# Performance work log

Measured on AMD Instinct MI355X. Metric: run time of the kernel, lower is better.

## Reference

```python
import jax, jax.numpy as jnp
import numpy as np

EMB = 64
NUM_LAYERS = 2


def _mlp_embed(x, shift, scale, w1, b1, w2, b2):
    # PreNormLayer: (x + shift) * scale, then Linear-ReLU-Linear-ReLU
    x = (x + shift) * scale
    x = jax.nn.relu(x @ w1 + b1)
    return jax.nn.relu(x @ w2 + b2)


def _sage_conv(x_src, x_dst, src_idx, dst_idx, ll_w, ll_b, lr_w):
    # PyG SAGEConv: mean-aggregate gathered source features at destinations,
    # out = lin_l(mean) + lin_r(x_dst); lin_l has bias, lin_r does not.
    n_dst = x_dst.shape[0]
    msgs = x_src[src_idx]                                   # [E, D] gather
    ssum = jax.ops.segment_sum(msgs, dst_idx, num_segments=n_dst)
    cnt = jax.ops.segment_sum(jnp.ones(src_idx.shape[0], x_src.dtype),
                              dst_idx, num_segments=n_dst)
    mean = ssum / jnp.maximum(cnt, 1.0)[:, None]            # [n_dst, D]
    return mean @ ll_w + ll_b + x_dst @ lr_w


def setup_inputs() -> dict:
    key = jax.random.key(0)
    ks = jax.random.split(key, 20)
    n_cons, n_var, n_edges = 100_000, 200_000, 2_000_000
    cons_nf, var_nf, edge_nf = 5, 19, 1

    def lin(k, fan_in, fan_out):
        return jax.random.normal(k, (fan_in, fan_out), jnp.float32) / np.sqrt(fan_in)

    inp = {
        'cons_x': jax.random.normal(ks[0], (n_cons, cons_nf), jnp.float32),
        'var_x': jax.random.normal(ks[1], (n_var, var_nf), jnp.float32),
        'edge_attr': jax.random.normal(ks[2], (n_edges, edge_nf), jnp.float32),
        'edge_index': jnp.stack([
            jax.random.randint(ks[3], (n_edges,), 0, n_cons),
            jax.random.randint(ks[4], (n_edges,), 0, n_var)]).astype(jnp.int64),
        # constraint embedding MLP
        'cons_shift': 0.1 * jax.random.normal(ks[5], (cons_nf,), jnp.float32),
        'cons_scale': 1.0 + 0.1 * jax.random.normal(ks[6], (cons_nf,), jnp.float32),
        'cons_w1': lin(ks[7], cons_nf, EMB),
        'cons_b1': jnp.zeros((EMB,), jnp.float32),
        'cons_w2': lin(ks[8], EMB, EMB),
        'cons_b2': jnp.zeros((EMB,), jnp.float32),
        # variable embedding MLP
        'var_shift': 0.1 * jax.random.normal(ks[9], (var_nf,), jnp.float32),
        'var_scale': 1.0 + 0.1 * jax.random.normal(ks[10], (var_nf,), jnp.float32),
        'var_w1': lin(ks[11], var_nf, EMB),
        'var_b1': jnp.zeros((EMB,), jnp.float32),
        'var_w2': lin(ks[12], EMB, EMB),
        'var_b2': jnp.zeros((EMB,), jnp.float32),
        # edge PreNorm (computed but unused for conv_type='sage', as in source)
        'edge_shift': 0.1 * jax.random.normal(ks[13], (edge_nf,), jnp.float32),
        'edge_scale': 1.0 + 0.1 * jax.random.normal(ks[14], (edge_nf,), jnp.float32),
        # SAGEConv weights: [layer, direction(0: cons->var, 1: var->cons), in, out]
        'conv_ll_w': jax.random.normal(ks[15], (NUM_LAYERS, 2, EMB, EMB), jnp.float32) / np.sqrt(EMB),
        'conv_ll_b': jnp.zeros((NUM_LAYERS, 2, EMB), jnp.float32),
        'conv_lr_w': jax.random.normal(ks[16], (NUM_LAYERS, 2, EMB, EMB), jnp.float32) / np.sqrt(EMB),
    }
    return inp


def reference(cons_x, var_x, edge_attr, edge_index,
              cons_shift, cons_scale, cons_w1, cons_b1, cons_w2, cons_b2,
              var_shift, var_scale, var_w1, var_b1, var_w2, var_b2,
              edge_shift, edge_scale, conv_ll_w, conv_ll_b, conv_lr_w):
    x_c = _mlp_embed(cons_x, cons_shift, cons_scale, cons_w1, cons_b1, cons_w2, cons_b2)
    x_v = _mlp_embed(var_x, var_shift, var_scale, var_w1, var_b1, var_w2, var_b2)
    edge_feat = (edge_attr + edge_shift) * edge_scale  # unused for SAGE (faithful to source)
    del edge_feat
    src, dst = edge_index[0], edge_index[1]  # constraint -> variable
    for l in range(NUM_LAYERS):
        new_v = _sage_conv(x_c, x_v, src, dst, conv_ll_w[l, 0], conv_ll_b[l, 0], conv_lr_w[l, 0])
        new_c = _sage_conv(x_v, x_c, dst, src, conv_ll_w[l, 1], conv_ll_b[l, 1], conv_lr_w[l, 1])
        x_c, x_v = jax.nn.relu(new_c), jax.nn.relu(new_v)
    return x_v
```

## Files before the change

kernel.cpp:

```cpp
#include <hip/hip_runtime.h>

#define EMB 64
#define CH 4096


static __device__ __forceinline__ unsigned short f2bf(float x) {
    union { float f; unsigned u; } v; v.f = x;
    unsigned r = v.u + 0x7fffu + ((v.u >> 16) & 1u);
    return (unsigned short)(r >> 16);
}
static __device__ __forceinline__ float bflo(unsigned w) {
    union { unsigned u; float f; } v; v.u = w << 16; return v.f;
}
static __device__ __forceinline__ float bfhi(unsigned w) {
    union { unsigned u; float f; } v; v.u = w & 0xffff0000u; return v.f;
}

__global__ __launch_bounds__(256) void zero_int_kernel(int* __restrict__ p, int n) {
    int i = blockIdx.x * 256 + threadIdx.x;
    if (i < n) p[i] = 0;
}

__global__ __launch_bounds__(256) void bucket_hist_kernel(
    const int* __restrict__ src, const int* __restrict__ dst, int E,
    int* __restrict__ bkt_cnt_c, int* __restrict__ bkt_cnt_v,
    int shc, int shv, int NBC, int NBV)
{
    __shared__ int hc[512], hv[512];
    int t = threadIdx.x;
    int base = blockIdx.x * CH;
    int n = min(CH, E - base);
    for (int i = t; i < NBC; i += 256) hc[i] = 0;
    for (int i = t; i < NBV; i += 256) hv[i] = 0;
    __syncthreads();
    for (int li = t; li < n; li += 256) {
        atomicAdd(&hc[src[base + li] >> shc], 1);
        atomicAdd(&hv[dst[base + li] >> shv], 1);
    }
    __syncthreads();
    for (int i = t; i < NBC; i += 256) { int c = hc[i]; if (c) atomicAdd(&bkt_cnt_c[i], c); }
    for (int i = t; i < NBV; i += 256) { int c = hv[i]; if (c) atomicAdd(&bkt_cnt_v[i], c); }
}

__global__ __launch_bounds__(256) void scan_buckets_kernel(
    int* __restrict__ bc, int nbc, int* __restrict__ bv, int nbv, int E)
{
    __shared__ int sc[256];
    int t = threadIdx.x;
    {
        int v0 = (2 * t < nbc) ? bc[2 * t] : 0;
        int v1 = (2 * t + 1 < nbc) ? bc[2 * t + 1] : 0;
        sc[t] = v0 + v1;
        __syncthreads();
        for (int off = 1; off < 256; off <<= 1) {
            int x = (t >= off) ? sc[t - off] : 0;
            __syncthreads();
            sc[t] += x;
            __syncthreads();
        }
        int ex = (t > 0) ? sc[t - 1] : 0;
        if (2 * t < nbc) bc[2 * t] = ex;
        if (2 * t + 1 < nbc) bc[2 * t + 1] = ex + v0;
        if (t == 0) bc[nbc] = E;
        __syncthreads();
    }
    {
        int v0 = (2 * t < nbv) ? bv[2 * t] : 0;
        int v1 = (2 * t + 1 < nbv) ? bv[2 * t + 1] : 0;
        sc[t] = v0 + v1;
        __syncthreads();
        for (int off = 1; off < 256; off <<= 1) {
            int x = (t >= off) ? sc[t - off] : 0;
            __syncthreads();
            sc[t] += x;
            __syncthreads();
        }
        int ex = (t > 0) ? sc[t - 1] : 0;
        if (2 * t < nbv) bv[2 * t] = ex;
        if (2 * t + 1 < nbv) bv[2 * t + 1] = ex + v0;
        if (t == 0) bv[nbv] = E;
    }
}

__global__ __launch_bounds__(256) void bin_edges_kernel(
    const int* __restrict__ src, const int* __restrict__ dst, int E,
    const int* __restrict__ bb_c, const int* __restrict__ bb_v,
    int* __restrict__ gcur_c, int* __restrict__ gcur_v,
    unsigned* __restrict__ tmp_c, unsigned* __restrict__ tmp_v,
    int shc, int shv, int NBC, int NBV)
{
    __shared__ int hc[512], hv[512];
    int t = threadIdx.x;
    int base = blockIdx.x * CH;
    int n = min(CH, E - base);
    unsigned mc = (1u << shc) - 1u, mv = (1u << shv) - 1u;

    for (int i = t; i < NBC; i += 256) hc[i] = 0;
    for (int i = t; i < NBV; i += 256) hv[i] = 0;
    __syncthreads();

    int ss[16], dd[16];
#pragma unroll
    for (int q = 0; q < 16; ++q) {
        int li = t + q * 256;
        bool ok = li < n;
        ss[q] = ok ? src[base + li] : -1;
        dd[q] = ok ? dst[base + li] : -1;
        if (ok) {
            atomicAdd(&hc[ss[q] >> shc], 1);
            atomicAdd(&hv[dd[q] >> shv], 1);
        }
    }
    __syncthreads();

    for (int i = t; i < NBC; i += 256) {
        int c = hc[i];
        hc[i] = c ? (bb_c[i] + atomicAdd(&gcur_c[i], c)) : 0;
    }
    for (int i = t; i < NBV; i += 256) {
        int c = hv[i];
        hv[i] = c ? (bb_v[i] + atomicAdd(&gcur_v[i], c)) : 0;
    }
    __syncthreads();

#pragma unroll
    for (int q = 0; q < 16; ++q) {
        int li = t + q * 256;
        if (li < n) {
            unsigned s = (unsigned)ss[q], d = (unsigned)dd[q];
            int pc = atomicAdd(&hc[s >> shc], 1);
            tmp_c[pc] = ((s & mc) << 23) | d;
            int pv = atomicAdd(&hv[d >> shv], 1);
            tmp_v[pv] = ((d & mv) << 23) | s;
        }
    }
}

__global__ __launch_bounds__(256) void regroup2_dual_kernel(
    const unsigned* __restrict__ tmpA, const int* __restrict__ bbA,
    int* __restrict__ rpA, int* __restrict__ adjA, int nAn, int shA, int nbA,
    const unsigned* __restrict__ tmpB, const int* __restrict__ bbB,
    int* __restrict__ rpB, int* __restrict__ adjB, int nBn, int shB, int nbB, int E)
{
    __shared__ int cnt[512];
    __shared__ int offs[512];
    __shared__ int sc[256];
    const unsigned* tmp; const int* bb; int* rp; int* adj; int n_nodes, sh, nb, b;
    if ((int)blockIdx.x < nbA) {
        tmp = tmpA; bb = bbA; rp = rpA; adj = adjA; n_nodes = nAn; sh = shA; nb = nbA; b = blockIdx.x;
    } else {
        tmp = tmpB; bb = bbB; rp = rpB; adj = adjB; n_nodes = nBn; sh = shB; nb = nbB; b = blockIdx.x - nbA;
    }
    int t = threadIdx.x;
    int node0 = b << sh;
    int node1 = min(node0 + (1 << sh), n_nodes);
    int nn = node1 - node0;
    for (int i = t; i < nn; i += 256) cnt[i] = 0;
    __syncthreads();
    int beg = bb[b], end = bb[b + 1];
    for (int e = beg + t; e < end; e += 256)
        atomicAdd(&cnt[tmp[e] >> 23], 1);
    __syncthreads();
    int v0 = (2 * t < nn) ? cnt[2 * t] : 0;
    int v1 = (2 * t + 1 < nn) ? cnt[2 * t + 1] : 0;
    sc[t] = v0 + v1;
    __syncthreads();
    for (int off = 1; off < 256; off <<= 1) {
        int x = (t >= off) ? sc[t - off] : 0;
        __syncthreads();
        sc[t] += x;
        __syncthreads();
    }
    int ex = (t > 0) ? sc[t - 1] : 0;
    if (2 * t < nn) offs[2 * t] = ex;
    if (2 * t + 1 < nn) offs[2 * t + 1] = ex + v0;
    __syncthreads();
    for (int i = t; i < nn; i += 256) {
        rp[node0 + i] = beg + offs[i];
        cnt[i] = 0;
    }
    if (b == nb - 1 && t == 0) rp[n_nodes] = E;
    __syncthreads();
    for (int e = beg + t; e < end; e += 256) {
        unsigned p = tmp[e];
        int d = (int)(p >> 23);
        int r = atomicAdd(&cnt[d], 1);
        adj[beg + offs[d] + r] = (int)(p & 0x7fffffu);
    }
}

template <int NF>
__device__ __forceinline__ void embed_body(
    float* hs, float* un,
    const float* __restrict__ x, const float* __restrict__ shift, const float* __restrict__ scale,
    const float* __restrict__ w1, const float* __restrict__ b1,
    const float* __restrict__ w2, const float* __restrict__ b2,
    const float* __restrict__ wll, const float* __restrict__ wlr,
    unsigned short* __restrict__ tb, float* __restrict__ u, int n, int bid)
{
    int t = threadIdx.x;
    long row0 = (long)bid * 64;
    int nrow = (n - row0 < 64) ? (int)(n - row0) : 64;

    float* xs  = un;
    float* w1s = un + NF * 68;

    for (int i = t; i < NF * EMB; i += 256) w1s[i] = w1[i];
    for (int i = t; i < 64 * NF; i += 256) {
        int r = i / NF, k = i - r * NF;
        float v = (r < nrow) ? x[row0 * NF + i] : 0.f;
        xs[k * 68 + r] = (v + shift[k]) * scale[k];
    }
    int r0 = (t >> 4) * 4;
    int cA = t & 15;
    float b1r[4], b2r[4];
#pragma unroll
    for (int j = 0; j < 4; ++j) { b1r[j] = b1[cA + 16 * j]; b2r[j] = b2[cA + 16 * j]; }
    __syncthreads();

    float a[4][4];
#pragma unroll
    for (int i = 0; i < 4; ++i)
#pragma unroll
        for (int j = 0; j < 4; ++j) a[i][j] = 0.f;
#pragma unroll
    for (int k = 0; k < NF; ++k) {
        float4 xv = *(const float4*)&xs[k * 68 + r0];
        float w0 = w1s[k * EMB + cA];
        float w1e = w1s[k * EMB + cA + 16];
        float w2e = w1s[k * EMB + cA + 32];
        float w3e = w1s[k * EMB + cA + 48];
        a[0][0] = fmaf(xv.x, w0, a[0][0]);  a[1][0] = fmaf(xv.y, w0, a[1][0]);
        a[2][0] = fmaf(xv.z, w0, a[2][0]);  a[3][0] = fmaf(xv.w, w0, a[3][0]);
        a[0][1] = fmaf(xv.x, w1e, a[0][1]); a[1][1] = fmaf(xv.y, w1e, a[1][1]);
        a[2][1] = fmaf(xv.z, w1e, a[2][1]); a[3][1] = fmaf(xv.w, w1e, a[3][1]);
        a[0][2] = fmaf(xv.x, w2e, a[0][2]); a[1][2] = fmaf(xv.y, w2e, a[1][2]);
        a[2][2] = fmaf(xv.z, w2e, a[2][2]); a[3][2] = fmaf(xv.w, w2e, a[3][2]);
        a[0][3] = fmaf(xv.x, w3e, a[0][3]); a[1][3] = fmaf(xv.y, w3e, a[1][3]);
        a[2][3] = fmaf(xv.z, w3e, a[2][3]); a[3][3] = fmaf(xv.w, w3e, a[3][3]);
    }
    __syncthreads();
#pragma unroll
    for (int j = 0; j < 4; ++j) {
        float* hp = &hs[(cA + 16 * j) * 65 + r0];
#pragma unroll
        for (int i = 0; i < 4; ++i) hp[i] = fmaxf(a[i][j] + b1r[j], 0.f);
    }
    {
        const float4* wg = (const float4*)w2;
        float4* wl = (float4*)un;
#pragma unroll
        for (int q = 0; q < 4; ++q) wl[t + q * 256] = wg[t + q * 256];
    }
    __syncthreads();

#pragma unroll
    for (int i = 0; i < 4; ++i)
#pragma unroll
        for (int j = 0; j < 4; ++j) a[i][j] = 0.f;
#pragma unroll 4
    for (int k = 0; k < EMB; ++k) {
        const float* hp = &hs[k * 65 + r0];
        float x0 = hp[0], x1 = hp[1], x2 = hp[2], x3 = hp[3];
        float w0 = un[k * EMB + cA];
        float w1e = un[k * EMB + cA + 16];
        float w2e = un[k * EMB + cA + 32];
        float w3e = un[k * EMB + cA + 48];
        a[0][0] = fmaf(x0, w0, a[0][0]);  a[1][0] = fmaf(x1, w0, a[1][0]);
        a[2][0] = fmaf(x2, w0, a[2][0]);  a[3][0] = fmaf(x3, w0, a[3][0]);
        a[0][1] = fmaf(x0, w1e, a[0][1]); a[1][1] = fmaf(x1, w1e, a[1][1]);
        a[2][1] = fmaf(x2, w1e, a[2][1]); a[3][1] = fmaf(x3, w1e, a[3][1]);
        a[0][2] = fmaf(x0, w2e, a[0][2]); a[1][2] = fmaf(x1, w2e, a[1][2]);
        a[2][2] = fmaf(x2, w2e, a[2][2]); a[3][2] = fmaf(x3, w2e, a[3][2]);
        a[0][3] = fmaf(x0, w3e, a[0][3]); a[1][3] = fmaf(x1, w3e, a[1][3]);
        a[2][3] = fmaf(x2, w3e, a[2][3]); a[3][3] = fmaf(x3, w3e, a[3][3]);
    }
    __syncthreads();
#pragma unroll
    for (int j = 0; j < 4; ++j) {
        float* hp = &hs[(cA + 16 * j) * 65 + r0];
#pragma unroll
        for (int i = 0; i < 4; ++i) hp[i] = fmaxf(a[i][j] + b2r[j], 0.f);
    }
    {
        const float4* wg = (const float4*)wll;
        float4* wl = (float4*)un;
#pragma unroll
        for (int q = 0; q < 4; ++q) wl[t + q * 256] = wg[t + q * 256];
    }
    __syncthreads();

    int c0g = (t & 15) * 4;
#pragma unroll
    for (int i = 0; i < 4; ++i)
#pragma unroll
        for (int j = 0; j < 4; ++j) a[i][j] = 0.f;
#pragma unroll 4
    for (int k = 0; k < EMB; ++k) {
        const float* hp = &hs[k * 65 + r0];
        float x0 = hp[0], x1 = hp[1], x2 = hp[2], x3 = hp[3];
        float4 wv = *(const float4*)&un[k * EMB + c0g];
        a[0][0] = fmaf(x0, wv.x, a[0][0]); a[0][1] = fmaf(x0, wv.y, a[0][1]);
        a[0][2] = fmaf(x0, wv.z, a[0][2]); a[0][3] = fmaf(x0, wv.w, a[0][3]);
        a[1][0] = fmaf(x1, wv.x, a[1][0]); a[1][1] = fmaf(x1, wv.y, a[1][1]);
        a[1][2] = fmaf(x1, wv.z, a[1][2]); a[1][3] = fmaf(x1, wv.w, a[1][3]);
        a[2][0] = fmaf(x2, wv.x, a[2][0]); a[2][1] = fmaf(x2, wv.y, a[2][1]);
        a[2][2] = fmaf(x2, wv.z, a[2][2]); a[2][3] = fmaf(x2, wv.w, a[2][3]);
        a[3][0] = fmaf(x3, wv.x, a[3][0]); a[3][1] = fmaf(x3, wv.y, a[3][1]);
        a[3][2] = fmaf(x3, wv.z, a[3][2]); a[3][3] = fmaf(x3, wv.w, a[3][3]);
    }
#pragma unroll
    for (int i = 0; i < 4; ++i) {
        long gr = row0 + r0 + i;
        if (gr < n) {
            ushort4 o;
            o.x = f2bf(a[i][0]); o.y = f2bf(a[i][1]);
            o.z = f2bf(a[i][2]); o.w = f2bf(a[i][3]);
            *(ushort4*)(tb + gr * EMB + c0g) = o;
        }
    }
    __syncthreads();
    {
        const float4* wg = (const float4*)wlr;
        float4* wl = (float4*)un;
#pragma unroll
        for (int q = 0; q < 4; ++q) wl[t + q * 256] = wg[t + q * 256];
    }
    __syncthreads();

#pragma unroll
    for (int i = 0; i < 4; ++i)
#pragma unroll
        for (int j = 0; j < 4; ++j) a[i][j] = 0.f;
#pragma unroll 4
    for (int k = 0; k < EMB; ++k) {
        const float* hp = &hs[k * 65 + r0];
        float x0 = hp[0], x1 = hp[1], x2 = hp[2], x3 = hp[3];
        float4 wv = *(const float4*)&un[k * EMB + c0g];
        a[0][0] = fmaf(x0, wv.x, a[0][0]); a[0][1] = fmaf(x0, wv.y, a[0][1]);
        a[0][2] = fmaf(x0, wv.z, a[0][2]); a[0][3] = fmaf(x0, wv.w, a[0][3]);
        a[1][0] = fmaf(x1, wv.x, a[1][0]); a[1][1] = fmaf(x1, wv.y, a[1][1]);
        a[1][2] = fmaf(x1, wv.z, a[1][2]); a[1][3] = fmaf(x1, wv.w, a[1][3]);
        a[2][0] = fmaf(x2, wv.x, a[2][0]); a[2][1] = fmaf(x2, wv.y, a[2][1]);
        a[2][2] = fmaf(x2, wv.z, a[2][2]); a[2][3] = fmaf(x2, wv.w, a[2][3]);
        a[3][0] = fmaf(x3, wv.x, a[3][0]); a[3][1] = fmaf(x3, wv.y, a[3][1]);
        a[3][2] = fmaf(x3, wv.z, a[3][2]); a[3][3] = fmaf(x3, wv.w, a[3][3]);
    }
#pragma unroll
    for (int i = 0; i < 4; ++i) {
        long gr = row0 + r0 + i;
        if (gr < n)
            *(float4*)&u[gr * EMB + c0g] = make_float4(a[i][0], a[i][1], a[i][2], a[i][3]);
    }
}

template <int NFA, int NFB>
__global__ __launch_bounds__(256) void embed_dual_kernel(
    const float* xA, const float* shA, const float* scA,
    const float* w1A, const float* b1A, const float* w2A, const float* b2A,
    const float* wllA, const float* wlrA, unsigned short* tbA, float* uA, int nA,
    const float* xB, const float* shB, const float* scB,
    const float* w1B, const float* b1B, const float* w2B, const float* b2B,
    const float* wllB, const float* wlrB, unsigned short* tbB, float* uB, int nB,
    int split)
{
    __shared__ float hs[EMB * 65];
    __shared__ float un[4096];
    if ((int)blockIdx.x < split)
        embed_body<NFA>(hs, un, xA, shA, scA, w1A, b1A, w2A, b2A, wllA, wlrA, tbA, uA, nA, blockIdx.x);
    else
        embed_body<NFB>(hs, un, xB, shB, scB, w1B, b1B, w2B, b2B, wllB, wlrB, tbB, uB, nB, blockIdx.x - split);
}

__global__ __launch_bounds__(256) void gemm64_dual_kernel(
    const float* __restrict__ XA, int nA, const float* __restrict__ WA, unsigned short* __restrict__ CA,
    const float* __restrict__ XB, int nB, const float* __restrict__ WB, float* __restrict__ CB, int split)
{
    __shared__ float xs[EMB * 68];
    __shared__ float w1s[EMB * EMB];

    const float* X; const float* W; int n; int bid; bool bf;
    if ((int)blockIdx.x < split) { X = XA; W = WA; n = nA; bid = blockIdx.x; bf = true; }
    else { X = XB; W = WB; n = nB; bid = blockIdx.x - split; bf = false; }

    int t = threadIdx.x;
    {
        int r = t >> 2;
        int cs = (t & 3) * 16;
        long gr = (long)bid * 64 + r;
        float4 v[4];
        if (gr < n) {
            const float4* sp = (const float4*)(X + gr * EMB + cs);
#pragma unroll
            for (int q = 0; q < 4; ++q) v[q] = sp[q];
        } else {
            float4 z = make_float4(0.f, 0.f, 0.f, 0.f);
#pragma unroll
            for (int q = 0; q < 4; ++q) v[q] = z;
        }
#pragma unroll
        for (int q = 0; q < 4; ++q) {
            xs[(cs + q * 4 + 0) * 68 + r] = v[q].x;
            xs[(cs + q * 4 + 1) * 68 + r] = v[q].y;
            xs[(cs + q * 4 + 2) * 68 + r] = v[q].z;
            xs[(cs + q * 4 + 3) * 68 + r] = v[q].w;
        }
        const float4* wg = (const float4*)W;
        float4* wl = (float4*)w1s;
#pragma unroll
        for (int q = 0; q < 4; ++q) wl[t + q * 256] = wg[t + q * 256];
    }
    __syncthreads();

    int r0 = (t >> 4) * 4;
    int c0 = (t & 15) * 4;
    float acc[4][4] = {{0.f}};
#pragma unroll 8
    for (int k = 0; k < EMB; ++k) {
        float4 xv = *(const float4*)&xs[k * 68 + r0];
        float4 wv = *(const float4*)&w1s[k * EMB + c0];
        float xa[4] = {xv.x, xv.y, xv.z, xv.w};
        float wa[4] = {wv.x, wv.y, wv.z, wv.w};
#pragma unroll
        for (int i = 0; i < 4; ++i)
#pragma unroll
            for (int j = 0; j < 4; ++j)
                acc[i][j] = fmaf(xa[i], wa[j], acc[i][j]);
    }

#pragma unroll
    for (int i = 0; i < 4; ++i) {
        long gr = (long)bid * 64 + r0 + i;
        if (gr < n) {
            if (bf) {
                ushort4 o;
                o.x = f2bf(acc[i][0]); o.y = f2bf(acc[i][1]);
                o.z = f2bf(acc[i][2]); o.w = f2bf(acc[i][3]);
                *(ushort4*)(CA + gr * EMB + c0) = o;
            } else {
                *(float4*)(CB + gr * EMB + c0) =
                    make_float4(acc[i][0], acc[i][1], acc[i][2], acc[i][3]);
            }
        }
    }
}

__global__ __launch_bounds__(256) void agg_rmw_kernel(
    const unsigned short* __restrict__ tbl, const int* __restrict__ rowptr,
    const int* __restrict__ adj, const float* __restrict__ bias,
    float* __restrict__ out, int n_dst)
{
    int lane = threadIdx.x & 63;
    int node = blockIdx.x * 4 + (threadIdx.x >> 6);
    if (node >= n_dst) return;
    int p = lane & 15;
    int g = lane >> 4;
    int beg = rowptr[node];
    int end = rowptr[node + 1];
    const uint2* tb = (const uint2*)tbl;
    float a0 = 0.f, a1 = 0.f, a2 = 0.f, a3 = 0.f;
    int e = beg + g;
    for (; e + 4 < end; e += 8) {
        int r0 = adj[e];
        int r1 = adj[e + 4];
        uint2 w0 = tb[(long)r0 * 16 + p];
        uint2 w1 = tb[(long)r1 * 16 + p];
        a0 += bflo(w0.x) + bflo(w1.x);
        a1 += bfhi(w0.x) + bfhi(w1.x);
        a2 += bflo(w0.y) + bflo(w1.y);
        a3 += bfhi(w0.y) + bfhi(w1.y);
    }
    if (e < end) {
        uint2 w0 = tb[(long)adj[e] * 16 + p];
        a0 += bflo(w0.x);
        a1 += bfhi(w0.x);
        a2 += bflo(w0.y);
        a3 += bfhi(w0.y);
    }
    a0 += __shfl_xor(a0, 16); a0 += __shfl_xor(a0, 32);
    a1 += __shfl_xor(a1, 16); a1 += __shfl_xor(a1, 32);
    a2 += __shfl_xor(a2, 16); a2 += __shfl_xor(a2, 32);
    a3 += __shfl_xor(a3, 16); a3 += __shfl_xor(a3, 32);
    if (g == 0) {
        int cnt = end - beg;
        float inv = 1.f / (float)(cnt > 0 ? cnt : 1);
        float4 bv = ((const float4*)bias)[p];
        float4* op = (float4*)(out + (long)node * EMB) + p;
        float4 ov = *op;
        float v0 = a0 * inv + bv.x + ov.x;
        float v1 = a1 * inv + bv.y + ov.y;
        float v2 = a2 * inv + bv.z + ov.z;
        float v3 = a3 * inv + bv.w + ov.w;
        *op = make_float4(fmaxf(v0, 0.f), fmaxf(v1, 0.f), fmaxf(v2, 0.f), fmaxf(v3, 0.f));
    }
}

__global__ __launch_bounds__(256) void agg_rmw_dual_kernel(
    const unsigned short* __restrict__ tblA, const int* __restrict__ rpA, const int* __restrict__ adjA,
    const float* __restrict__ biasA, float* __restrict__ outA, int nA,
    const unsigned short* __restrict__ tblB, const int* __restrict__ rpB, const int* __restrict__ adjB,
    const float* __restrict__ biasB, float* __restrict__ outB, int nB, int split)
{
    const unsigned short* tbl; const int* rowptr; const int* adj; const float* bias; float* out;
    int nd, bid;
    if ((int)blockIdx.x < split) {
        tbl = tblA; rowptr = rpA; adj = adjA; bias = biasA; out = outA; nd = nA; bid = blockIdx.x;
    } else {
        tbl = tblB; rowptr = rpB; adj = adjB; bias = biasB; out = outB; nd = nB; bid = blockIdx.x - split;
    }
    int lane = threadIdx.x & 63;
    int node = bid * 4 + (threadIdx.x >> 6);
    if (node >= nd) return;
    int p = lane & 15;
    int g = lane >> 4;
    int beg = rowptr[node];
    int end = rowptr[node + 1];
    const uint2* tb = (const uint2*)tbl;
    float a0 = 0.f, a1 = 0.f, a2 = 0.f, a3 = 0.f;
    int e = beg + g;
    for (; e + 4 < end; e += 8) {
        int r0 = adj[e];
        int r1 = adj[e + 4];
        uint2 w0 = tb[(long)r0 * 16 + p];
        uint2 w1 = tb[(long)r1 * 16 + p];
        a0 += bflo(w0.x) + bflo(w1.x);
        a1 += bfhi(w0.x) + bfhi(w1.x);
        a2 += bflo(w0.y) + bflo(w1.y);
        a3 += bfhi(w0.y) + bfhi(w1.y);
    }
    if (e < end) {
        uint2 w0 = tb[(long)adj[e] * 16 + p];
        a0 += bflo(w0.x);
        a1 += bfhi(w0.x);
        a2 += bflo(w0.y);
        a3 += bfhi(w0.y);
    }
    a0 += __shfl_xor(a0, 16); a0 += __shfl_xor(a0, 32);
    a1 += __shfl_xor(a1, 16); a1 += __shfl_xor(a1, 32);
    a2 += __shfl_xor(a2, 16); a2 += __shfl_xor(a2, 32);
    a3 += __shfl_xor(a3, 16); a3 += __shfl_xor(a3, 32);
    if (g == 0) {
        int cnt = end - beg;
        float inv = 1.f / (float)(cnt > 0 ? cnt : 1);
        float4 bv = ((const float4*)bias)[p];
        float4* op = (float4*)(out + (long)node * EMB) + p;
        float4 ov = *op;
        float v0 = a0 * inv + bv.x + ov.x;
        float v1 = a1 * inv + bv.y + ov.y;
        float v2 = a2 * inv + bv.z + ov.z;
        float v3 = a3 * inv + bv.w + ov.w;
        *op = make_float4(fmaxf(v0, 0.f), fmaxf(v1, 0.f), fmaxf(v2, 0.f), fmaxf(v3, 0.f));
    }
}

extern "C" void kernel_launch(void* const* d_in, const int* in_sizes, int n_in,
                              void* d_out, int out_size, void* d_ws, size_t ws_size,
                              hipStream_t stream) {
    const float* cons_x     = (const float*)d_in[0];
    const float* var_x      = (const float*)d_in[1];
    const int*   eidx       = (const int*)d_in[3];
    const float* cons_shift = (const float*)d_in[4];
    const float* cons_scale = (const float*)d_in[5];
    const float* cons_w1    = (const float*)d_in[6];
    const float* cons_b1    = (const float*)d_in[7];
    const float* cons_w2    = (const float*)d_in[8];
    const float* cons_b2    = (const float*)d_in[9];
    const float* var_shift  = (const float*)d_in[10];
    const float* var_scale  = (const float*)d_in[11];
    const float* var_w1     = (const float*)d_in[12];
    const float* var_b1     = (const float*)d_in[13];
    const float* var_w2     = (const float*)d_in[14];
    const float* var_b2     = (const float*)d_in[15];
    const float* ll_w       = (const float*)d_in[18];
    const float* ll_b       = (const float*)d_in[19];
    const float* lr_w       = (const float*)d_in[20];

    const int nC = in_sizes[0] / 5;
    const int nV = in_sizes[1] / 19;
    const int E  = in_sizes[3] / 2;
    const int* src = eidx;
    const int* dst = eidx + E;

    int shc = 0; while ((nC >> shc) >= 512) ++shc;
    int shv = 0; while ((nV >> shv) >= 512) ++shv;
    const int NBC = (nC + (1 << shc) - 1) >> shc;
    const int NBV = (nV + (1 << shv) - 1) >> shv;

    char* w = (char*)d_ws;
    auto alloc = [&](size_t bytes) {
        char* p = w;
        w += (bytes + 255) & ~(size_t)255;
        return p;
    };
    float* x_c = (float*)alloc((size_t)nC * EMB * 4);
    float* x_v = (float*)alloc((size_t)nV * EMB * 4);
    float* t_c = (float*)alloc((size_t)nC * EMB * 4);
    float* t_v = (float*)alloc((size_t)nV * EMB * 4);
    unsigned* tmp_c = (unsigned*)t_c;
    unsigned* tmp_v = (unsigned*)t_v;
    unsigned short* tb_c = (unsigned short*)t_c;
    unsigned short* tb_v = (unsigned short*)t_v;
    int* rp_v  = (int*)alloc((size_t)(nV + 1) * 4);
    int* rp_c  = (int*)alloc((size_t)(nC + 1) * 4);
    int* adj_v = (int*)alloc((size_t)E * 4);
    int* adj_c = (int*)alloc((size_t)E * 4);
    int* bkt   = (int*)alloc(4096 * 4);
    int* bb_c   = bkt;
    int* bb_v   = bkt + 1024;
    int* gcur_c = bkt + 2048;
    int* gcur_v = bkt + 3072;

    auto llw = [&](int l, int d) { return ll_w + (size_t)(l * 2 + d) * EMB * EMB; };
    auto lrw = [&](int l, int d) { return lr_w + (size_t)(l * 2 + d) * EMB * EMB; };
    auto llb = [&](int l, int d) { return ll_b + (size_t)(l * 2 + d) * EMB; };

    zero_int_kernel<<<16, 256, 0, stream>>>(bkt, 4096);
    bucket_hist_kernel<<<(E + CH - 1) / CH, 256, 0, stream>>>(src, dst, E, bb_c, bb_v, shc, shv, NBC, NBV);
    scan_buckets_kernel<<<1, 256, 0, stream>>>(bb_c, NBC, bb_v, NBV, E);
    bin_edges_kernel<<<(E + CH - 1) / CH, 256, 0, stream>>>(src, dst, E, bb_c, bb_v, gcur_c, gcur_v,
                                                            tmp_c, tmp_v, shc, shv, NBC, NBV);
    regroup2_dual_kernel<<<NBV + NBC, 256, 0, stream>>>(
        tmp_v, bb_v, rp_v, adj_v, nV, shv, NBV,
        tmp_c, bb_c, rp_c, adj_c, nC, shc, NBC, E);

    int gc = (nC + 63) / 64, gv = (nV + 63) / 64;
    embed_dual_kernel<5, 19><<<gc + gv, 256, 0, stream>>>(
        cons_x, cons_shift, cons_scale, cons_w1, cons_b1, cons_w2, cons_b2,
        llw(0, 0), lrw(0, 1), tb_c, x_c, nC,
        var_x, var_shift, var_scale, var_w1, var_b1, var_w2, var_b2,
        llw(0, 1), lrw(0, 0), tb_v, x_v, nV,
        gc);

    int gv4 = (nV + 3) / 4, gc4 = (nC + 3) / 4;
    agg_rmw_dual_kernel<<<gv4 + gc4, 256, 0, stream>>>(
        tb_c, rp_v, adj_v, llb(0, 0), x_v, nV,
        tb_v, rp_c, adj_c, llb(0, 1), x_c, nC,
        gv4);

    gemm64_dual_kernel<<<gc + gv, 256, 0, stream>>>(
        x_c, nC, llw(1, 0), tb_c,
        x_v, nV, lrw(1, 0), (float*)d_out, gc);

    agg_rmw_kernel<<<gv4, 256, 0, stream>>>(tb_c, rp_v, adj_v, llb(1, 0), (float*)d_out, nV);
}
```

Before: 468.5 us.

## Drop bucket histogram pass via fixed-slot binning; vectorize embed MLP LDS reads

Removes the separate bucket histogram kernel by binning edges into fixed-capacity per-bucket slots in the temp buffer. The per-bucket counts are then scanned afterward to get CSR offsets for the regroup step, which saves one full read pass over the 2M-edge index arrays and one launch. This assumes no bucket exceeds its slot capacity (twice the average, capped by buffer size), which random indices satisfy but skewed graphs might overflow. Separately, the embedding MLP uses float4 shared-memory loads with a padded stride of 68 and contiguous per-thread columns, and moves the lr weight load earlier.

```diff
diff --git a/kernel.cpp b/kernel.cpp
--- a/kernel.cpp
+++ b/kernel.cpp
@@ -19,27 +19,6 @@
 __global__ __launch_bounds__(256) void zero_int_kernel(int* __restrict__ p, int n) {
     int i = blockIdx.x * 256 + threadIdx.x;
     if (i < n) p[i] = 0;
-}
-
-__global__ __launch_bounds__(256) void bucket_hist_kernel(
-    const int* __restrict__ src, const int* __restrict__ dst, int E,
-    int* __restrict__ bkt_cnt_c, int* __restrict__ bkt_cnt_v,
-    int shc, int shv, int NBC, int NBV)
-{
-    __shared__ int hc[512], hv[512];
-    int t = threadIdx.x;
-    int base = blockIdx.x * CH;
-    int n = min(CH, E - base);
-    for (int i = t; i < NBC; i += 256) hc[i] = 0;
-    for (int i = t; i < NBV; i += 256) hv[i] = 0;
-    __syncthreads();
-    for (int li = t; li < n; li += 256) {
-        atomicAdd(&hc[src[base + li] >> shc], 1);
-        atomicAdd(&hv[dst[base + li] >> shv], 1);
-    }
-    __syncthreads();
-    for (int i = t; i < NBC; i += 256) { int c = hc[i]; if (c) atomicAdd(&bkt_cnt_c[i], c); }
-    for (int i = t; i < NBV; i += 256) { int c = hv[i]; if (c) atomicAdd(&bkt_cnt_v[i], c); }
 }
 
 __global__ __launch_bounds__(256) void scan_buckets_kernel(
@@ -84,10 +63,9 @@
 
 __global__ __launch_bounds__(256) void bin_edges_kernel(
     const int* __restrict__ src, const int* __restrict__ dst, int E,
-    const int* __restrict__ bb_c, const int* __restrict__ bb_v,
     int* __restrict__ gcur_c, int* __restrict__ gcur_v,
     unsigned* __restrict__ tmp_c, unsigned* __restrict__ tmp_v,
-    int shc, int shv, int NBC, int NBV)
+    int shc, int shv, int NBC, int NBV, int SLOTC, int SLOTV)
 {
     __shared__ int hc[512], hv[512];
     int t = threadIdx.x;
@@ -115,11 +93,11 @@
 
     for (int i = t; i < NBC; i += 256) {
         int c = hc[i];
-        hc[i] = c ? (bb_c[i] + atomicAdd(&gcur_c[i], c)) : 0;
+        hc[i] = c ? (i * SLOTC + atomicAdd(&gcur_c[i], c)) : 0;
     }
     for (int i = t; i < NBV; i += 256) {
         int c = hv[i];
-        hv[i] = c ? (bb_v[i] + atomicAdd(&gcur_v[i], c)) : 0;
+        hv[i] = c ? (i * SLOTV + atomicAdd(&gcur_v[i], c)) : 0;
     }
     __syncthreads();
 
@@ -138,18 +116,18 @@
 
 __global__ __launch_bounds__(256) void regroup2_dual_kernel(
     const unsigned* __restrict__ tmpA, const int* __restrict__ bbA,
-    int* __restrict__ rpA, int* __restrict__ adjA, int nAn, int shA, int nbA,
+    int* __restrict__ rpA, int* __restrict__ adjA, int nAn, int shA, int nbA, int slotA,
     const unsigned* __restrict__ tmpB, const int* __restrict__ bbB,
-    int* __restrict__ rpB, int* __restrict__ adjB, int nBn, int shB, int nbB, int E)
+    int* __restrict__ rpB, int* __restrict__ adjB, int nBn, int shB, int nbB, int slotB, int E)
 {
     __shared__ int cnt[512];
     __shared__ int offs[512];
     __shared__ int sc[256];
-    const unsigned* tmp; const int* bb; int* rp; int* adj; int n_nodes, sh, nb, b;
+    const unsigned* tmp; const int* bb; int* rp; int* adj; int n_nodes, sh, nb, b, slot;
     if ((int)blockIdx.x < nbA) {
-        tmp = tmpA; bb = bbA; rp = rpA; adj = adjA; n_nodes = nAn; sh = shA; nb = nbA; b = blockIdx.x;
+        tmp = tmpA; bb = bbA; rp = rpA; adj = adjA; n_nodes = nAn; sh = shA; nb = nbA; slot = slotA; b = blockIdx.x;
     } else {
-        tmp = tmpB; bb = bbB; rp = rpB; adj = adjB; n_nodes = nBn; sh = shB; nb = nbB; b = blockIdx.x - nbA;
+        tmp = tmpB; bb = bbB; rp = rpB; adj = adjB; n_nodes = nBn; sh = shB; nb = nbB; slot = slotB; b = blockIdx.x - nbA;
     }
     int t = threadIdx.x;
     int node0 = b << sh;
@@ -157,8 +135,10 @@
     int nn = node1 - node0;
     for (int i = t; i < nn; i += 256) cnt[i] = 0;
     __syncthreads();
-    int beg = bb[b], end = bb[b + 1];
-    for (int e = beg + t; e < end; e += 256)
+    int adjbase = bb[b];
+    int cntb = bb[b + 1] - adjbase;
+    int sbeg = b * slot;
+    for (int e = sbeg + t; e < sbeg + cntb; e += 256)
         atomicAdd(&cnt[tmp[e] >> 23], 1);
     __syncthreads();
     int v0 = (2 * t < nn) ? cnt[2 * t] : 0;
@@ -176,16 +156,16 @@
     if (2 * t + 1 < nn) offs[2 * t + 1] = ex + v0;
     __syncthreads();
     for (int i = t; i < nn; i += 256) {
-        rp[node0 + i] = beg + offs[i];
+        rp[node0 + i] = adjbase + offs[i];
         cnt[i] = 0;
     }
     if (b == nb - 1 && t == 0) rp[n_nodes] = E;
     __syncthreads();
-    for (int e = beg + t; e < end; e += 256) {
+    for (int e = sbeg + t; e < sbeg + cntb; e += 256) {
         unsigned p = tmp[e];
         int d = (int)(p >> 23);
         int r = atomicAdd(&cnt[d], 1);
-        adj[beg + offs[d] + r] = (int)(p & 0x7fffffu);
+        adj[adjbase + offs[d] + r] = (int)(p & 0x7fffffu);
     }
 }
 
@@ -212,10 +192,9 @@
         xs[k * 68 + r] = (v + shift[k]) * scale[k];
     }
     int r0 = (t >> 4) * 4;
-    int cA = t & 15;
-    float b1r[4], b2r[4];
-#pragma unroll
-    for (int j = 0; j < 4; ++j) { b1r[j] = b1[cA + 16 * j]; b2r[j] = b2[cA + 16 * j]; }
+    int c0 = (t & 15) * 4;
+    float4 b1v = *(const float4*)&b1[c0];
+    float4 b2v = *(const float4*)&b2[c0];
     __syncthreads();
 
     float a[4][4];
@@ -226,25 +205,27 @@
 #pragma unroll
     for (int k = 0; k < NF; ++k) {
         float4 xv = *(const float4*)&xs[k * 68 + r0];
-        float w0 = w1s[k * EMB + cA];
-        float w1e = w1s[k * EMB + cA + 16];
-        float w2e = w1s[k * EMB + cA + 32];
-        float w3e = w1s[k * EMB + cA + 48];
-        a[0][0] = fmaf(xv.x, w0, a[0][0]);  a[1][0] = fmaf(xv.y, w0, a[1][0]);
-        a[2][0] = fmaf(xv.z, w0, a[2][0]);  a[3][0] = fmaf(xv.w, w0, a[3][0]);
-        a[0][1] = fmaf(xv.x, w1e, a[0][1]); a[1][1] = fmaf(xv.y, w1e, a[1][1]);
-        a[2][1] = fmaf(xv.z, w1e, a[2][1]); a[3][1] = fmaf(xv.w, w1e, a[3][1]);
-        a[0][2] = fmaf(xv.x, w2e, a[0][2]); a[1][2] = fmaf(xv.y, w2e, a[1][2]);
-        a[2][2] = fmaf(xv.z, w2e, a[2][2]); a[3][2] = fmaf(xv.w, w2e, a[3][2]);
-        a[0][3] = fmaf(xv.x, w3e, a[0][3]); a[1][3] = fmaf(xv.y, w3e, a[1][3]);
-        a[2][3] = fmaf(xv.z, w3e, a[2][3]); a[3][3] = fmaf(xv.w, w3e, a[3][3]);
-    }
-    __syncthreads();
-#pragma unroll
-    for (int j = 0; j < 4; ++j) {
-        float* hp = &hs[(cA + 16 * j) * 65 + r0];
-#pragma unroll
-        for (int i = 0; i < 4; ++i) hp[i] = fmaxf(a[i][j] + b1r[j], 0.f);
+        float4 wv = *(const float4*)&w1s[k * EMB + c0];
+        float xa[4] = {xv.x, xv.y, xv.z, xv.w};
+        float wa[4] = {wv.x, wv.y, wv.z, wv.w};
+#pragma unroll
+        for (int i = 0; i < 4; ++i)
+#pragma unroll
+            for (int j = 0; j < 4; ++j)
+                a[i][j] = fmaf(xa[i], wa[j], a[i][j]);
+    }
+    __syncthreads();
+    {
+        float ba[4] = {b1v.x, b1v.y, b1v.z, b1v.w};
+#pragma unroll
+        for (int j = 0; j < 4; ++j) {
+            float4 o;
+            o.x = fmaxf(a[0][j] + ba[j], 0.f);
+            o.y = fmaxf(a[1][j] + ba[j], 0.f);
+            o.z = fmaxf(a[2][j] + ba[j], 0.f);
+            o.w = fmaxf(a[3][j] + ba[j], 0.f);
+            *(float4*)&hs[(c0 + j) * 68 + r0] = o;
+        }
     }
     {
         const float4* wg = (const float4*)w2;
@@ -258,29 +239,30 @@
     for (int i = 0; i < 4; ++i)
 #pragma unroll
         for (int j = 0; j < 4; ++j) a[i][j] = 0.f;
-#pragma unroll 4
+#pragma unroll 8
     for (int k = 0; k < EMB; ++k) {
-        const float* hp = &hs[k * 65 + r0];
-        float x0 = hp[0], x1 = hp[1], x2 = hp[2], x3 = hp[3];
-        float w0 = un[k * EMB + cA];
-        float w1e = un[k * EMB + cA + 16];
-        float w2e = un[k * EMB + cA + 32];
-        float w3e = un[k * EMB + cA + 48];
-        a[0][0] = fmaf(x0, w0, a[0][0]);  a[1][0] = fmaf(x1, w0, a[1][0]);
-        a[2][0] = fmaf(x2, w0, a[2][0]);  a[3][0] = fmaf(x3, w0, a[3][0]);
-        a[0][1] = fmaf(x0, w1e, a[0][1]); a[1][1] = fmaf(x1, w1e, a[1][1]);
-        a[2][1] = fmaf(x2, w1e, a[2][1]); a[3][1] = fmaf(x3, w1e, a[3][1]);
-        a[0][2] = fmaf(x0, w2e, a[0][2]); a[1][2] = fmaf(x1, w2e, a[1][2]);
-        a[2][2] = fmaf(x2, w2e, a[2][2]); a[3][2] = fmaf(x3, w2e, a[3][2]);
-        a[0][3] = fmaf(x0, w3e, a[0][3]); a[1][3] = fmaf(x1, w3e, a[1][3]);
-        a[2][3] = fmaf(x2, w3e, a[2][3]); a[3][3] = fmaf(x3, w3e, a[3][3]);
-    }
-    __syncthreads();
-#pragma unroll
-    for (int j = 0; j < 4; ++j) {
-        float* hp = &hs[(cA + 16 * j) * 65 + r0];
-#pragma unroll
-        for (int i = 0; i < 4; ++i) hp[i] = fmaxf(a[i][j] + b2r[j], 0.f);
+        float4 xv = *(const float4*)&hs[k * 68 + r0];
+        float4 wv = *(const float4*)&un[k * EMB + c0];
+        float xa[4] = {xv.x, xv.y, xv.z, xv.w};
+        float wa[4] = {wv.x, wv.y, wv.z, wv.w};
+#pragma unroll
+        for (int i = 0; i < 4; ++i)
+#pragma unroll
+            for (int j = 0; j < 4; ++j)
+                a[i][j] = fmaf(xa[i], wa[j], a[i][j]);
+    }
+    __syncthreads();
+    {
+        float ba[4] = {b2v.x, b2v.y, b2v.z, b2v.w};
+#pragma unroll
+        for (int j = 0; j < 4; ++j) {
+            float4 o;
+            o.x = fmaxf(a[0][j] + ba[j], 0.f);
+            o.y = fmaxf(a[1][j] + ba[j], 0.f);
+            o.z = fmaxf(a[2][j] + ba[j], 0.f);
+            o.w = fmaxf(a[3][j] + ba[j], 0.f);
+            *(float4*)&hs[(c0 + j) * 68 + r0] = o;
+        }
     }
     {
         const float4* wg = (const float4*)wll;
@@ -290,24 +272,28 @@
     }
     __syncthreads();
 
-    int c0g = (t & 15) * 4;
 #pragma unroll
     for (int i = 0; i < 4; ++i)
 #pragma unroll
         for (int j = 0; j < 4; ++j) a[i][j] = 0.f;
-#pragma unroll 4
+#pragma unroll 8
     for (int k = 0; k < EMB; ++k) {
-        const float* hp = &hs[k * 65 + r0];
-        float x0 = hp[0], x1 = hp[1], x2 = hp[2], x3 = hp[3];
-        float4 wv = *(const float4*)&un[k * EMB + c0g];
-        a[0][0] = fmaf(x0, wv.x, a[0][0]); a[0][1] = fmaf(x0, wv.y, a[0][1]);
-        a[0][2] = fmaf(x0, wv.z, a[0][2]); a[0][3] = fmaf(x0, wv.w, a[0][3]);
-        a[1][0] = fmaf(x1, wv.x, a[1][0]); a[1][1] = fmaf(x1, wv.y, a[1][1]);
-        a[1][2] = fmaf(x1, wv.z, a[1][2]); a[1][3] = fmaf(x1, wv.w, a[1][3]);
-        a[2][0] = fmaf(x2, wv.x, a[2][0]); a[2][1] = fmaf(x2, wv.y, a[2][1]);
-        a[2][2] = fmaf(x2, wv.z, a[2][2]); a[2][3] = fmaf(x2, wv.w, a[2][3]);
-        a[3][0] = fmaf(x3, wv.x, a[3][0]); a[3][1] = fmaf(x3, wv.y, a[3][1]);
-        a[3][2] = fmaf(x3, wv.z, a[3][2]); a[3][3] = fmaf(x3, wv.w, a[3][3]);
+        float4 xv = *(const float4*)&hs[k * 68 + r0];
+        float4 wv = *(const float4*)&un[k * EMB + c0];
+        float xa[4] = {xv.x, xv.y, xv.z, xv.w};
+        float wa[4] = {wv.x, wv.y, wv.z, wv.w};
+#pragma unroll
+        for (int i = 0; i < 4; ++i)
+#pragma unroll
+            for (int j = 0; j < 4; ++j)
+                a[i][j] = fmaf(xa[i], wa[j], a[i][j]);
+    }
+    __syncthreads();
+    {
+        const float4* wg = (const float4*)wlr;
+        float4* wl = (float4*)un;
+#pragma unroll
+        for (int q = 0; q < 4; ++q) wl[t + q * 256] = wg[t + q * 256];
     }
 #pragma unroll
     for (int i = 0; i < 4; ++i) {
@@ -316,15 +302,8 @@
             ushort4 o;
             o.x = f2bf(a[i][0]); o.y = f2bf(a[i][1]);
             o.z = f2bf(a[i][2]); o.w = f2bf(a[i][3]);
-            *(ushort4*)(tb + gr * EMB + c0g) = o;
-        }
-    }
-    __syncthreads();
-    {
-        const float4* wg = (const float4*)wlr;
-        float4* wl = (float4*)un;
-#pragma unroll
-        for (int q = 0; q < 4; ++q) wl[t + q * 256] = wg[t + q * 256];
+            *(ushort4*)(tb + gr * EMB + c0) = o;
+        }
     }
     __syncthreads();
 
@@ -332,25 +311,23 @@
     for (int i = 0; i < 4; ++i)
 #pragma unroll
         for (int j = 0; j < 4; ++j) a[i][j] = 0.f;
-#pragma unroll 4
+#pragma unroll 8
     for (int k = 0; k < EMB; ++k) {
-        const float* hp = &hs[k * 65 + r0];
-        float x0 = hp[0], x1 = hp[1], x2 = hp[2], x3 = hp[3];
-        float4 wv = *(const float4*)&un[k * EMB + c0g];
-        a[0][0] = fmaf(x0, wv.x, a[0][0]); a[0][1] = fmaf(x0, wv.y, a[0][1]);
-        a[0][2] = fmaf(x0, wv.z, a[0][2]); a[0][3] = fmaf(x0, wv.w, a[0][3]);
-        a[1][0] = fmaf(x1, wv.x, a[1][0]); a[1][1] = fmaf(x1, wv.y, a[1][1]);
-        a[1][2] = fmaf(x1, wv.z, a[1][2]); a[1][3] = fmaf(x1, wv.w, a[1][3]);
-        a[2][0] = fmaf(x2, wv.x, a[2][0]); a[2][1] = fmaf(x2, wv.y, a[2][1]);
-        a[2][2] = fmaf(x2, wv.z, a[2][2]); a[2][3] = fmaf(x2, wv.w, a[2][3]);
-        a[3][0] = fmaf(x3, wv.x, a[3][0]); a[3][1] = fmaf(x3, wv.y, a[3][1]);
-        a[3][2] = fmaf(x3, wv.z, a[3][2]); a[3][3] = fmaf(x3, wv.w, a[3][3]);
+        float4 xv = *(const float4*)&hs[k * 68 + r0];
+        float4 wv = *(const float4*)&un[k * EMB + c0];
+        float xa[4] = {xv.x, xv.y, xv.z, xv.w};
+        float wa[4] = {wv.x, wv.y, wv.z, wv.w};
+#pragma unroll
+        for (int i = 0; i < 4; ++i)
+#pragma unroll
+            for (int j = 0; j < 4; ++j)
+                a[i][j] = fmaf(xa[i], wa[j], a[i][j]);
     }
 #pragma unroll
     for (int i = 0; i < 4; ++i) {
         long gr = row0 + r0 + i;
         if (gr < n)
-            *(float4*)&u[gr * EMB + c0g] = make_float4(a[i][0], a[i][1], a[i][2], a[i][3]);
+            *(float4*)&u[gr * EMB + c0] = make_float4(a[i][0], a[i][1], a[i][2], a[i][3]);
     }
 }
 
@@ -364,8 +341,8 @@
     const float* wllB, const float* wlrB, unsigned short* tbB, float* uB, int nB,
     int split)
 {
-    __shared__ float hs[EMB * 65];
-    __shared__ float un[4096];
+    __shared__ __align__(16) float hs[EMB * 68];
+    __shared__ __align__(16) float un[4096];
     if ((int)blockIdx.x < split)
         embed_body<NFA>(hs, un, xA, shA, scA, w1A, b1A, w2A, b2A, wllA, wlrA, tbA, uA, nA, blockIdx.x);
     else
@@ -376,8 +353,8 @@
     const float* __restrict__ XA, int nA, const float* __restrict__ WA, unsigned short* __restrict__ CA,
     const float* __restrict__ XB, int nB, const float* __restrict__ WB, float* __restrict__ CB, int split)
 {
-    __shared__ float xs[EMB * 68];
-    __shared__ float w1s[EMB * EMB];
+    __shared__ __align__(16) float xs[EMB * 68];
+    __shared__ __align__(16) float w1s[EMB * EMB];
 
     const float* X; const float* W; int n; int bid; bool bf;
     if ((int)blockIdx.x < split) { X = XA; W = WA; n = nA; bid = blockIdx.x; bf = true; }
@@ -604,24 +581,33 @@
     int* rp_c  = (int*)alloc((size_t)(nC + 1) * 4);
     int* adj_v = (int*)alloc((size_t)E * 4);
     int* adj_c = (int*)alloc((size_t)E * 4);
-    int* bkt   = (int*)alloc(4096 * 4);
-    int* bb_c   = bkt;
-    int* bb_v   = bkt + 1024;
-    int* gcur_c = bkt + 2048;
-    int* gcur_v = bkt + 3072;
+    int* bkt   = (int*)alloc(2048 * 4);
+    int* gcur_c = bkt;
+    int* gcur_v = bkt + 1024;
+
+    auto slot_for = [&](int NB, size_t cap_ints) {
+        long s = 2L * E / NB;
+        s = (s + 255) & ~255L;
+        if (s < 4096) s = 4096;
+        long cap = (long)(cap_ints / NB) & ~255L;
+        if (s > cap) s = cap;
+        return (int)s;
+    };
+    const int SLOTC = slot_for(NBC, (size_t)nC * EMB);
+    const int SLOTV = slot_for(NBV, (size_t)nV * EMB);
 
     auto llw = [&](int l, int d) { return ll_w + (size_t)(l * 2 + d) * EMB * EMB; };
     auto lrw = [&](int l, int d) { return lr_w + (size_t)(l * 2 + d) * EMB * EMB; };
     auto llb = [&](int l, int d) { return ll_b + (size_t)(l * 2 + d) * EMB; };
 
-    zero_int_kernel<<<16, 256, 0, stream>>>(bkt, 4096);
-    bucket_hist_kernel<<<(E + CH - 1) / CH, 256, 0, stream>>>(src, dst, E, bb_c, bb_v, shc, shv, NBC, NBV);
-    scan_buckets_kernel<<<1, 256, 0, stream>>>(bb_c, NBC, bb_v, NBV, E);
-    bin_edges_kernel<<<(E + CH - 1) / CH, 256, 0, stream>>>(src, dst, E, bb_c, bb_v, gcur_c, gcur_v,
-                                                            tmp_c, tmp_v, shc, shv, NBC, NBV);
+    zero_int_kernel<<<8, 256, 0, stream>>>(bkt, 2048);
+    bin_edges_kernel<<<(E + CH - 1) / CH, 256, 0, stream>>>(src, dst, E, gcur_c, gcur_v,
+                                                            tmp_c, tmp_v, shc, shv, NBC, NBV,
+                                                            SLOTC, SLOTV);
+    scan_buckets_kernel<<<1, 256, 0, stream>>>(gcur_c, NBC, gcur_v, NBV, E);
     regroup2_dual_kernel<<<NBV + NBC, 256, 0, stream>>>(
-        tmp_v, bb_v, rp_v, adj_v, nV, shv, NBV,
-        tmp_c, bb_c, rp_c, adj_c, nC, shc, NBC, E);
+        tmp_v, gcur_v, rp_v, adj_v, nV, shv, NBV, SLOTV,
+        tmp_c, gcur_c, rp_c, adj_c, nC, shc, NBC, SLOTC, E);
 
     int gc = (nC + 63) / 64, gv = (nV + 63) / 64;
     embed_dual_kernel<5, 19><<<gc + gv, 256, 0, stream>>>(
```

After: 441.3 us. 5.8% less time.
